# Kernel optimization log

Hardware: AMD Instinct MI355X
Metric: run time of the kernel (lower is better)

## Reference

```python
import math
import jax, jax.numpy as jnp
import numpy as np

B, Q, M = 4, 512, 8192
LOC_D, SENS_D, EMB_D = 8, 256, 512


def setup_inputs() -> dict:
    key = jax.random.key(0)
    ks = jax.random.split(key, 6)
    location = jax.random.normal(ks[0], (B, Q, LOC_D), dtype=jnp.float32)
    # sds must be positive (they are squared and logged); keep them away from 0
    location_sd = jax.random.uniform(ks[1], (B, Q, LOC_D), dtype=jnp.float32) * 0.9 + 0.1
    memory_locations = jax.random.normal(ks[2], (B, M, LOC_D), dtype=jnp.float32)
    memory_location_sds = jax.random.uniform(ks[3], (B, M, LOC_D), dtype=jnp.float32) * 0.9 + 0.1
    memory_senses = jax.random.normal(ks[4], (B, M, EMB_D), dtype=jnp.float32)
    # sensory_read_proj: Linear(embed_dim -> sensory_dim, bias=False)
    W_read = jax.random.normal(ks[5], (SENS_D, EMB_D), dtype=jnp.float32) / math.sqrt(EMB_D)
    return {
        "location": location,
        "location_sd": location_sd,
        "memory_locations": memory_locations,
        "memory_location_sds": memory_location_sds,
        "memory_senses": memory_senses,
        "W_read": W_read,
    }


def reference(location, location_sd, memory_locations, memory_location_sds, memory_senses, W_read):
    # BidirectionalMemory.read with match_threshold=None, detach_* True (stop_gradient)
    mem_loc = jax.lax.stop_gradient(memory_locations)
    mem_sd = jax.lax.stop_gradient(memory_location_sds)
    mem_sense = jax.lax.stop_gradient(memory_senses)

    # (B,Q,1,D) - (B,1,M,D) -> (B,Q,M,D)
    delta = location[:, :, None, :] - mem_loc[:, None, :, :]
    var = location_sd[:, :, None, :] ** 2 + mem_sd[:, None, :, :] ** 2
    d = delta.shape[-1]
    # -0.5 * sum((delta^2 / (var+eps))^2) - 0.5*log(2pi)*D - sum(log(var))
    log_aff = (
        -0.5 * jnp.sum((delta ** 2 / (var + 1e-8)) ** 2, axis=-1)
        - 0.5 * math.log(2.0 * math.pi) * d
        - jnp.sum(jnp.log(var), axis=-1)
    )  # (B,Q,M)
    weights = jax.nn.softmax(log_aff, axis=-1)  # (B,Q,M)
    pre_sense = jnp.einsum("bqm,bme->bqe", weights, mem_sense)  # (B,Q,EMB_D)
    sense = jnp.einsum("bqe,se->bqs", pre_sense, W_read)  # (B,Q,SENS_D)
    return sense
```

## Files before the change

kernel.cpp:

```cpp
#include <hip/hip_runtime.h>
#include <hip/hip_bf16.h>

#define BB 4
#define QQ 512
#define MM 8192
#define DD 8
#define EE 512
#define SS 256

#define QG 16
#define MSP 8
#define MSL (MM / MSP)
#define NQG (BB * QQ / QG)

using f32x4  = __attribute__((ext_vector_type(4))) float;
using bf16x8 = __attribute__((ext_vector_type(8))) short;

static __device__ __forceinline__ unsigned short f2bf(float f) {
  union { __hip_bfloat16 h; unsigned short u; } v;
  v.h = __float2bfloat16(f);
  return v.u;
}

__global__ __launch_bounds__(256) void k_proj(
    const float* __restrict__ V, const float* __restrict__ W,
    unsigned short* __restrict__ projT)
{
  const int m0 = blockIdx.x * 128;
  const int s0 = blockIdx.y * 128;
  const int b  = blockIdx.z;
  const int t = threadIdx.x, lane = t & 63, wv = t >> 6;
  const int wr = wv >> 1, wc = wv & 1;

  __shared__ short lA[128 * 64];
  __shared__ short lB[128 * 64];

  f32x4 acc[4][4] = {};

  const float* Wp = W + (size_t)s0 * EE;
  const float* Vp = V + (size_t)b * MM * EE + (size_t)m0 * EE;

  const int r0 = t >> 4;
  const int c0 = (t & 15) * 4;
  const int swz = (r0 & 7) << 3;

  float4 ra[8], rb[8];

#define P_LOADS(K0)                                                        \
  _Pragma("unroll")                                                        \
  for (int j = 0; j < 8; ++j) {                                            \
    const int row = j * 16 + r0;                                           \
    ra[j] = *reinterpret_cast<const float4*>(&Wp[(size_t)row * EE + (K0) + c0]); \
    rb[j] = *reinterpret_cast<const float4*>(&Vp[(size_t)row * EE + (K0) + c0]); \
  }

  P_LOADS(0)

  for (int ki = 0; ki < 8; ++ki) {
    __syncthreads();
#pragma unroll
    for (int j = 0; j < 8; ++j) {
      const int row = j * 16 + r0;
      const int idx = (row * 64 + c0) ^ swz;
      ushort4 da, db;
      da.x = f2bf(ra[j].x); da.y = f2bf(ra[j].y); da.z = f2bf(ra[j].z); da.w = f2bf(ra[j].w);
      db.x = f2bf(rb[j].x); db.y = f2bf(rb[j].y); db.z = f2bf(rb[j].z); db.w = f2bf(rb[j].w);
      *reinterpret_cast<ushort4*>(&lA[idx]) = da;
      *reinterpret_cast<ushort4*>(&lB[idx]) = db;
    }
    if (ki < 7) { P_LOADS((ki + 1) * 64) }
    __syncthreads();

#pragma unroll
    for (int kk = 0; kk < 2; ++kk) {
      const int kofs = kk * 32 + (lane >> 4) * 8;
      const int r15 = lane & 15;
      bf16x8 af[4], bfv[4];
#pragma unroll
      for (int mi = 0; mi < 4; ++mi) {
        int row = wr * 64 + mi * 16 + r15;
        af[mi] = *reinterpret_cast<const bf16x8*>(&lA[(row * 64 + kofs) ^ ((row & 7) << 3)]);
      }
#pragma unroll
      for (int ni = 0; ni < 4; ++ni) {
        int row = wc * 64 + ni * 16 + r15;
        bfv[ni] = *reinterpret_cast<const bf16x8*>(&lB[(row * 64 + kofs) ^ ((row & 7) << 3)]);
      }
#pragma unroll
      for (int mi = 0; mi < 4; ++mi)
#pragma unroll
        for (int ni = 0; ni < 4; ++ni)
          acc[mi][ni] = __builtin_amdgcn_mfma_f32_16x16x32_bf16(af[mi], bfv[ni], acc[mi][ni], 0, 0, 0);
    }
  }
#undef P_LOADS

  unsigned short* outp = projT + (size_t)b * SS * MM;
  const int fr = (lane >> 4) * 4;
  const int fc = lane & 15;
#pragma unroll
  for (int mi = 0; mi < 4; ++mi)
#pragma unroll
    for (int ni = 0; ni < 4; ++ni)
#pragma unroll
      for (int r = 0; r < 4; ++r) {
        int s = s0 + wr * 64 + mi * 16 + fr + r;
        int m = m0 + wc * 64 + ni * 16 + fc;
        outp[(size_t)s * MM + m] = f2bf(acc[mi][ni][r]);
      }
}

__global__ __launch_bounds__(512, 4) void k_fused(
    const float* __restrict__ loc, const float* __restrict__ locsd,
    const float* __restrict__ mloc, const float* __restrict__ msd,
    const unsigned short* __restrict__ projT,
    float* __restrict__ opart, float* __restrict__ mn_g,
    float* __restrict__ sum_g)
{
  __shared__ unsigned short p_s[QG * MSL];
  __shared__ float lx_s[QG][DD], ls2_s[QG][DD];
  __shared__ float redmin[QG][8];
  __shared__ float redsum[QG][8];

  const int hw = blockIdx.x;
  const int ms = hw & 7;
  const int qg = hw >> 3;
  const int b  = qg >> 5;
  const int q0 = (qg & 31) * QG;
  const int t = threadIdx.x, lane = t & 63, wv = t >> 6;

  if (t < QG * DD) {
    const int qq = t >> 3, d = t & 7;
    const int base = (b * QQ + q0 + qq) * DD + d;
    lx_s[qq][d] = loc[base];
    float s = locsd[base];
    ls2_s[qq][d] = __builtin_fmaf(s, s, 1e-8f);
  }

  const float4* ml4 = reinterpret_cast<const float4*>(mloc + (size_t)b * MM * DD);
  const float4* ms4 = reinterpret_cast<const float4*>(msd  + (size_t)b * MM * DD);
  float mlv[2][DD], ms2[2][DD];
#pragma unroll
  for (int p = 0; p < 2; ++p) {
    const int m = ms * MSL + 2 * t + p;
    float4 a0 = ml4[2 * m], a1 = ml4[2 * m + 1];
    float4 s0 = ms4[2 * m], s1 = ms4[2 * m + 1];
    mlv[p][0] = a0.x; mlv[p][1] = a0.y; mlv[p][2] = a0.z; mlv[p][3] = a0.w;
    mlv[p][4] = a1.x; mlv[p][5] = a1.y; mlv[p][6] = a1.z; mlv[p][7] = a1.w;
    ms2[p][0] = s0.x * s0.x; ms2[p][1] = s0.y * s0.y;
    ms2[p][2] = s0.z * s0.z; ms2[p][3] = s0.w * s0.w;
    ms2[p][4] = s1.x * s1.x; ms2[p][5] = s1.y * s1.y;
    ms2[p][6] = s1.z * s1.z; ms2[p][7] = s1.w * s1.w;
  }
  __syncthreads();

  const size_t g_base = ((size_t)qg * MSP + ms) * QG;

#pragma unroll
  for (int sub = 0; sub < 2; ++sub) {
    float la_r[8][2];
#pragma unroll
    for (int q8 = 0; q8 < 8; ++q8) {
      const int q = sub * 8 + q8;
      float lxq[DD], lsq[DD];
#pragma unroll
      for (int d = 0; d < DD; d += 4) {
        float4 v1 = *reinterpret_cast<const float4*>(&lx_s[q][d]);
        lxq[d] = v1.x; lxq[d + 1] = v1.y; lxq[d + 2] = v1.z; lxq[d + 3] = v1.w;
        float4 v2 = *reinterpret_cast<const float4*>(&ls2_s[q][d]);
        lsq[d] = v2.x; lsq[d + 1] = v2.y; lsq[d + 2] = v2.z; lsq[d + 3] = v2.w;
      }
      float mnq = 3.4e38f;
#pragma unroll
      for (int p = 0; p < 2; ++p) {
        float ssum = 0.f, pr = 1.f;
#pragma unroll
        for (int d = 0; d < DD; ++d) {
          float v  = lsq[d] + ms2[p][d];
          float r  = __builtin_amdgcn_rcpf(v);
          float dl = lxq[d] - mlv[p][d];
          float d2 = dl * dl;
          float tt = d2 * r;
          ssum = __builtin_fmaf(tt, tt, ssum);
          pr *= v;
        }
        la_r[q8][p] = __builtin_fmaf(ssum, 0.72134752f, __builtin_amdgcn_logf(pr));
        mnq = fminf(mnq, la_r[q8][p]);
      }
#pragma unroll
      for (int off = 32; off; off >>= 1) mnq = fminf(mnq, __shfl_xor(mnq, off, 64));
      if (lane == 0) redmin[q][wv] = mnq;
    }
    __syncthreads();
    float mnb[8];
#pragma unroll
    for (int q8 = 0; q8 < 8; ++q8) {
      const int q = sub * 8 + q8;
      float m2 = redmin[q][0];
#pragma unroll
      for (int w = 1; w < 8; ++w) m2 = fminf(m2, redmin[q][w]);
      mnb[q8] = m2;
      if (t == q8) mn_g[g_base + q] = m2;
    }
#pragma unroll
    for (int q8 = 0; q8 < 8; ++q8) {
      const int q = sub * 8 + q8;
      const int swz = (q & 7) << 4;
      float e0 = __builtin_amdgcn_exp2f(mnb[q8] - la_r[q8][0]);
      float e1 = __builtin_amdgcn_exp2f(mnb[q8] - la_r[q8][1]);
      unsigned int pk = (unsigned int)f2bf(e0) | ((unsigned int)f2bf(e1) << 16);
      *reinterpret_cast<unsigned int*>(
          (char*)p_s + (((q * MSL + 2 * t) * 2) ^ swz)) = pk;
      float v = e0 + e1;
#pragma unroll
      for (int off = 32; off; off >>= 1) v += __shfl_xor(v, off, 64);
      if (lane == 0) redsum[q][wv] = v;
    }
  }

  __syncthreads();
  if (t < QG) {
    float s = 0.f;
#pragma unroll
    for (int w = 0; w < 8; ++w) s += redsum[t][w];
    sum_g[g_base + t] = s;
  }

  const unsigned short* pTb = projT + (size_t)b * SS * MM + (size_t)ms * MSL;
  const int s0w = wv * 32;
  const int qf = lane & 15;
  const int kf = (lane >> 4) * 8;
  const int aswz = (qf & 7) << 4;
  f32x4 acc[2] = {};

#define LDA(CH) (*reinterpret_cast<const bf16x8*>( \
    (const char*)p_s + (((qf * MSL + (CH) * 32 + kf) * 2) ^ aswz)))
#define LOADB(U, CH)                                                        \
  _Pragma("unroll")                                                         \
  for (int ni = 0; ni < 2; ++ni)                                            \
    U[ni] = *reinterpret_cast<const uint4*>(                                \
        pTb + (size_t)(s0w + ni * 16 + qf) * MM + (CH) * 32 + kf);

  uint4 u0[2], u1[2];
  bf16x8 a0, a1;
  LOADB(u0, 0) a0 = LDA(0);
#pragma unroll 2
  for (int ch = 0; ch < 32; ch += 2) {
    LOADB(u1, ch + 1) a1 = LDA(ch + 1);
#pragma unroll
    for (int ni = 0; ni < 2; ++ni)
      acc[ni] = __builtin_amdgcn_mfma_f32_16x16x32_bf16(
          a0, *reinterpret_cast<const bf16x8*>(&u0[ni]), acc[ni], 0, 0, 0);
    if (ch + 2 < 32) { LOADB(u0, ch + 2) a0 = LDA(ch + 2); }
#pragma unroll
    for (int ni = 0; ni < 2; ++ni)
      acc[ni] = __builtin_amdgcn_mfma_f32_16x16x32_bf16(
          a1, *reinterpret_cast<const bf16x8*>(&u1[ni]), acc[ni], 0, 0, 0);
  }
#undef LDA
#undef LOADB

  float* op = opart + g_base * SS;
#pragma unroll
  for (int ni = 0; ni < 2; ++ni)
#pragma unroll
    for (int r = 0; r < 4; ++r) {
      const int q = (lane >> 4) * 4 + r;
      const int s = s0w + ni * 16 + qf;
      op[q * SS + s] = acc[ni][r];
    }
}

__global__ __launch_bounds__(256) void k_merge(
    const float* __restrict__ opart, const float* __restrict__ mn_g,
    const float* __restrict__ sum_g, float* __restrict__ out)
{
  const int row = blockIdx.x * 4 + (threadIdx.x >> 6);
  const int lane = threadIdx.x & 63;
  const int qg = row >> 4, q = row & 15;

  const float* mnp = mn_g  + (size_t)qg * MSP * QG + q;
  const float* smp = sum_g + (size_t)qg * MSP * QG + q;
  float mns[MSP], gmn = 3.4e38f;
#pragma unroll
  for (int i = 0; i < MSP; ++i) { mns[i] = mnp[i * QG]; gmn = fminf(gmn, mns[i]); }
  float gsum = 0.f, sc[MSP];
#pragma unroll
  for (int i = 0; i < MSP; ++i) {
    sc[i] = __builtin_amdgcn_exp2f(gmn - mns[i]);
    gsum = __builtin_fmaf(smp[i * QG], sc[i], gsum);
  }
  float o[4] = {0.f, 0.f, 0.f, 0.f};
  const float* ob = opart + (size_t)qg * MSP * (QG * SS) + q * SS;
#pragma unroll
  for (int i = 0; i < MSP; ++i)
#pragma unroll
    for (int j = 0; j < 4; ++j)
      o[j] = __builtin_fmaf(ob[(size_t)i * (QG * SS) + j * 64 + lane], sc[i], o[j]);
  const float inv = 1.0f / gsum;
  float* orow = out + (size_t)row * SS;
#pragma unroll
  for (int j = 0; j < 4; ++j) orow[j * 64 + lane] = o[j] * inv;
}


extern "C" void kernel_launch(void* const* d_in, const int* in_sizes, int n_in,
                              void* d_out, int out_size, void* d_ws, size_t ws_size,
                              hipStream_t stream) {
  const float* loc    = (const float*)d_in[0];
  const float* locsd  = (const float*)d_in[1];
  const float* mloc   = (const float*)d_in[2];
  const float* msd    = (const float*)d_in[3];
  const float* msense = (const float*)d_in[4];
  const float* wread  = (const float*)d_in[5];
  float* out = (float*)d_out;

  const size_t proj_bytes  = (size_t)BB * SS * MM * 2;
  const size_t opart_bytes = (size_t)NQG * MSP * QG * SS * 4;
  const size_t mn_bytes    = (size_t)NQG * MSP * QG * 4;
  if (ws_size < proj_bytes + opart_bytes + 2 * mn_bytes) return;

  unsigned short* projT = (unsigned short*)d_ws;
  float* opart = (float*)((char*)d_ws + proj_bytes);
  float* mn_g  = (float*)((char*)d_ws + proj_bytes + opart_bytes);
  float* sum_g = (float*)((char*)d_ws + proj_bytes + opart_bytes + mn_bytes);

  hipLaunchKernelGGL(k_proj, dim3(MM / 128, SS / 128, BB), dim3(256), 0, stream,
                     msense, wread, projT);
  hipLaunchKernelGGL(k_fused, dim3(NQG * MSP), dim3(512), 0, stream,
                     loc, locsd, mloc, msd, projT, opart, mn_g, sum_g);
  hipLaunchKernelGGL(k_merge, dim3(BB * QQ / 4), dim3(256), 0, stream,
                     opart, mn_g, sum_g, out);
}
```

Measured before the change: 111.1 us.

## Remap affinity stage so each half-wave owns one query

Threads are remapped so that each 32-lane half-wave handles one query and iterates over all memory slots of the slice, instead of each thread owning two memory slots across all 16 queries. This lets the per-query min and sum be reduced with in-wave shuffles only, removing the shared-memory reduction arrays and the intermediate block barriers. The per-dimension reciprocals are also replaced by two reciprocals of partial products, using shared sub-products to cut transcendental work. In exchange, memory location and sd data are now reloaded from global memory once per query (16x more global/L2 traffic), and the product-based reciprocal may lose precision.

```diff
diff --git a/kernel.cpp b/kernel.cpp
--- a/kernel.cpp
+++ b/kernel.cpp
@@ -12,6 +12,8 @@
 #define MSP 8
 #define MSL (MM / MSP)
 #define NQG (BB * QQ / QG)
+
+#define L2E 0.72134752f
 
 using f32x4  = __attribute__((ext_vector_type(4))) float;
 using bf16x8 = __attribute__((ext_vector_type(8))) short;
@@ -118,9 +120,7 @@
     float* __restrict__ sum_g)
 {
   __shared__ unsigned short p_s[QG * MSL];
-  __shared__ float lx_s[QG][DD], ls2_s[QG][DD];
-  __shared__ float redmin[QG][8];
-  __shared__ float redsum[QG][8];
+  __shared__ float2 lxls_s[QG][DD];
 
   const int hw = blockIdx.x;
   const int ms = hw & 7;
@@ -128,103 +128,90 @@
   const int b  = qg >> 5;
   const int q0 = (qg & 31) * QG;
   const int t = threadIdx.x, lane = t & 63, wv = t >> 6;
+  const int ql = t >> 5;
+  const int lh = lane & 31;
 
   if (t < QG * DD) {
     const int qq = t >> 3, d = t & 7;
     const int base = (b * QQ + q0 + qq) * DD + d;
-    lx_s[qq][d] = loc[base];
     float s = locsd[base];
-    ls2_s[qq][d] = __builtin_fmaf(s, s, 1e-8f);
-  }
+    float2 v; v.x = loc[base]; v.y = __builtin_fmaf(s, s, 1e-8f);
+    lxls_s[qq][d] = v;
+  }
+  __syncthreads();
+
+  float lx[DD], ls[DD];
+#pragma unroll
+  for (int d = 0; d < DD; ++d) {
+    float2 v = lxls_s[ql][d];
+    lx[d] = v.x; ls[d] = v.y;
+  }
+
+  const size_t g_base = ((size_t)qg * MSP + ms) * QG;
 
   const float4* ml4 = reinterpret_cast<const float4*>(mloc + (size_t)b * MM * DD);
   const float4* ms4 = reinterpret_cast<const float4*>(msd  + (size_t)b * MM * DD);
-  float mlv[2][DD], ms2[2][DD];
-#pragma unroll
-  for (int p = 0; p < 2; ++p) {
-    const int m = ms * MSL + 2 * t + p;
-    float4 a0 = ml4[2 * m], a1 = ml4[2 * m + 1];
-    float4 s0 = ms4[2 * m], s1 = ms4[2 * m + 1];
-    mlv[p][0] = a0.x; mlv[p][1] = a0.y; mlv[p][2] = a0.z; mlv[p][3] = a0.w;
-    mlv[p][4] = a1.x; mlv[p][5] = a1.y; mlv[p][6] = a1.z; mlv[p][7] = a1.w;
-    ms2[p][0] = s0.x * s0.x; ms2[p][1] = s0.y * s0.y;
-    ms2[p][2] = s0.z * s0.z; ms2[p][3] = s0.w * s0.w;
-    ms2[p][4] = s1.x * s1.x; ms2[p][5] = s1.y * s1.y;
-    ms2[p][6] = s1.z * s1.z; ms2[p][7] = s1.w * s1.w;
-  }
+  const int mb = ms * MSL + 2 * lh;
+
+  float la[16][2];
+  float mn = 3.4e38f;
+#pragma unroll
+  for (int i = 0; i < 16; ++i) {
+#pragma unroll
+    for (int p = 0; p < 2; ++p) {
+      const int m = mb + i * 64 + p;
+      float4 a0 = ml4[2 * m], a1 = ml4[2 * m + 1];
+      float4 s0 = ms4[2 * m], s1 = ms4[2 * m + 1];
+      float vv0 = ls[0] + s0.x * s0.x, vv1 = ls[1] + s0.y * s0.y;
+      float vv2 = ls[2] + s0.z * s0.z, vv3 = ls[3] + s0.w * s0.w;
+      float vv4 = ls[4] + s1.x * s1.x, vv5 = ls[5] + s1.y * s1.y;
+      float vv6 = ls[6] + s1.z * s1.z, vv7 = ls[7] + s1.w * s1.w;
+      float d0 = lx[0] - a0.x, d1 = lx[1] - a0.y, d2 = lx[2] - a0.z, d3 = lx[3] - a0.w;
+      float d4 = lx[4] - a1.x, d5 = lx[5] - a1.y, d6 = lx[6] - a1.z, d7 = lx[7] - a1.w;
+      float e0 = d0 * d0, e1 = d1 * d1, e2 = d2 * d2, e3 = d3 * d3;
+      float e4 = d4 * d4, e5 = d5 * d5, e6 = d6 * d6, e7 = d7 * d7;
+      float v01 = vv0 * vv1, v23 = vv2 * vv3, v45 = vv4 * vv5, v67 = vv6 * vv7;
+      float pA = v01 * v23, pB = v45 * v67;
+      float rA = __builtin_amdgcn_rcpf(pA);
+      float rB = __builtin_amdgcn_rcpf(pB);
+      float pp = pA * pB;
+      float t0 = e0 * vv1 * v23 * rA, t1 = e1 * vv0 * v23 * rA;
+      float t2 = e2 * vv3 * v01 * rA, t3 = e3 * vv2 * v01 * rA;
+      float t4 = e4 * vv5 * v67 * rB, t5 = e5 * vv4 * v67 * rB;
+      float t6 = e6 * vv7 * v45 * rB, t7 = e7 * vv6 * v45 * rB;
+      float ss = t0 * t0;
+      ss = __builtin_fmaf(t1, t1, ss);
+      ss = __builtin_fmaf(t2, t2, ss);
+      ss = __builtin_fmaf(t3, t3, ss);
+      ss = __builtin_fmaf(t4, t4, ss);
+      ss = __builtin_fmaf(t5, t5, ss);
+      ss = __builtin_fmaf(t6, t6, ss);
+      ss = __builtin_fmaf(t7, t7, ss);
+      la[i][p] = __builtin_fmaf(ss, L2E, __builtin_amdgcn_logf(pp));
+      mn = fminf(mn, la[i][p]);
+    }
+  }
+
+#pragma unroll
+  for (int off = 16; off; off >>= 1) mn = fminf(mn, __shfl_xor(mn, off, 64));
+  if (lh == 0) mn_g[g_base + ql] = mn;
+
+  const int swz = (ql & 7) << 4;
+  float sum = 0.f;
+#pragma unroll
+  for (int i = 0; i < 16; ++i) {
+    float e0 = __builtin_amdgcn_exp2f(mn - la[i][0]);
+    float e1 = __builtin_amdgcn_exp2f(mn - la[i][1]);
+    sum += e0 + e1;
+    unsigned int pk = (unsigned int)f2bf(e0) | ((unsigned int)f2bf(e1) << 16);
+    *reinterpret_cast<unsigned int*>(
+        (char*)p_s + (((ql * MSL + i * 64 + 2 * lh) * 2) ^ swz)) = pk;
+  }
+#pragma unroll
+  for (int off = 16; off; off >>= 1) sum += __shfl_xor(sum, off, 64);
+  if (lh == 0) sum_g[g_base + ql] = sum;
+
   __syncthreads();
-
-  const size_t g_base = ((size_t)qg * MSP + ms) * QG;
-
-#pragma unroll
-  for (int sub = 0; sub < 2; ++sub) {
-    float la_r[8][2];
-#pragma unroll
-    for (int q8 = 0; q8 < 8; ++q8) {
-      const int q = sub * 8 + q8;
-      float lxq[DD], lsq[DD];
-#pragma unroll
-      for (int d = 0; d < DD; d += 4) {
-        float4 v1 = *reinterpret_cast<const float4*>(&lx_s[q][d]);
-        lxq[d] = v1.x; lxq[d + 1] = v1.y; lxq[d + 2] = v1.z; lxq[d + 3] = v1.w;
-        float4 v2 = *reinterpret_cast<const float4*>(&ls2_s[q][d]);
-        lsq[d] = v2.x; lsq[d + 1] = v2.y; lsq[d + 2] = v2.z; lsq[d + 3] = v2.w;
-      }
-      float mnq = 3.4e38f;
-#pragma unroll
-      for (int p = 0; p < 2; ++p) {
-        float ssum = 0.f, pr = 1.f;
-#pragma unroll
-        for (int d = 0; d < DD; ++d) {
-          float v  = lsq[d] + ms2[p][d];
-          float r  = __builtin_amdgcn_rcpf(v);
-          float dl = lxq[d] - mlv[p][d];
-          float d2 = dl * dl;
-          float tt = d2 * r;
-          ssum = __builtin_fmaf(tt, tt, ssum);
-          pr *= v;
-        }
-        la_r[q8][p] = __builtin_fmaf(ssum, 0.72134752f, __builtin_amdgcn_logf(pr));
-        mnq = fminf(mnq, la_r[q8][p]);
-      }
-#pragma unroll
-      for (int off = 32; off; off >>= 1) mnq = fminf(mnq, __shfl_xor(mnq, off, 64));
-      if (lane == 0) redmin[q][wv] = mnq;
-    }
-    __syncthreads();
-    float mnb[8];
-#pragma unroll
-    for (int q8 = 0; q8 < 8; ++q8) {
-      const int q = sub * 8 + q8;
-      float m2 = redmin[q][0];
-#pragma unroll
-      for (int w = 1; w < 8; ++w) m2 = fminf(m2, redmin[q][w]);
-      mnb[q8] = m2;
-      if (t == q8) mn_g[g_base + q] = m2;
-    }
-#pragma unroll
-    for (int q8 = 0; q8 < 8; ++q8) {
-      const int q = sub * 8 + q8;
-      const int swz = (q & 7) << 4;
-      float e0 = __builtin_amdgcn_exp2f(mnb[q8] - la_r[q8][0]);
-      float e1 = __builtin_amdgcn_exp2f(mnb[q8] - la_r[q8][1]);
-      unsigned int pk = (unsigned int)f2bf(e0) | ((unsigned int)f2bf(e1) << 16);
-      *reinterpret_cast<unsigned int*>(
-          (char*)p_s + (((q * MSL + 2 * t) * 2) ^ swz)) = pk;
-      float v = e0 + e1;
-#pragma unroll
-      for (int off = 32; off; off >>= 1) v += __shfl_xor(v, off, 64);
-      if (lane == 0) redsum[q][wv] = v;
-    }
-  }
-
-  __syncthreads();
-  if (t < QG) {
-    float s = 0.f;
-#pragma unroll
-    for (int w = 0; w < 8; ++w) s += redsum[t][w];
-    sum_g[g_base + t] = s;
-  }
 
   const unsigned short* pTb = projT + (size_t)b * SS * MM + (size_t)ms * MSL;
   const int s0w = wv * 32;
```

Measured after the change: 142.3 us. +28.1%, slower.

## Split memory axis into 16 slices with one memory row per thread

Applied to the files above, without the earlier changes.

Doubles the number of memory-axis splits per query group, so each block handles half as many memory rows (one per thread instead of two) and the MFMA k-loop is halved. This gives twice as many blocks and smaller per-block LDS use, which may raise occupancy and parallelism. It also restructures the affinity pass into one sweep over all 16 queries with a shared-memory broadcast of the per-query minimum, replacing the two-half pass. The cost is twice as many partial outputs for the merge kernel to read and combine, plus more global traffic for the partial results.

```diff
diff --git a/kernel.cpp b/kernel.cpp
--- a/kernel.cpp
+++ b/kernel.cpp
@@ -9,9 +9,11 @@
 #define SS 256
 
 #define QG 16
-#define MSP 8
+#define MSP 16
 #define MSL (MM / MSP)
 #define NQG (BB * QQ / QG)
+
+#define L2E 0.72134752f
 
 using f32x4  = __attribute__((ext_vector_type(4))) float;
 using bf16x8 = __attribute__((ext_vector_type(8))) short;
@@ -121,10 +123,11 @@
   __shared__ float lx_s[QG][DD], ls2_s[QG][DD];
   __shared__ float redmin[QG][8];
   __shared__ float redsum[QG][8];
+  __shared__ float mnb_s[QG];
 
   const int hw = blockIdx.x;
-  const int ms = hw & 7;
-  const int qg = hw >> 3;
+  const int ms = hw & 15;
+  const int qg = hw >> 4;
   const int b  = qg >> 5;
   const int q0 = (qg & 31) * QG;
   const int t = threadIdx.x, lane = t & 63, wv = t >> 6;
@@ -139,85 +142,83 @@
 
   const float4* ml4 = reinterpret_cast<const float4*>(mloc + (size_t)b * MM * DD);
   const float4* ms4 = reinterpret_cast<const float4*>(msd  + (size_t)b * MM * DD);
-  float mlv[2][DD], ms2[2][DD];
-#pragma unroll
-  for (int p = 0; p < 2; ++p) {
-    const int m = ms * MSL + 2 * t + p;
-    float4 a0 = ml4[2 * m], a1 = ml4[2 * m + 1];
-    float4 s0 = ms4[2 * m], s1 = ms4[2 * m + 1];
-    mlv[p][0] = a0.x; mlv[p][1] = a0.y; mlv[p][2] = a0.z; mlv[p][3] = a0.w;
-    mlv[p][4] = a1.x; mlv[p][5] = a1.y; mlv[p][6] = a1.z; mlv[p][7] = a1.w;
-    ms2[p][0] = s0.x * s0.x; ms2[p][1] = s0.y * s0.y;
-    ms2[p][2] = s0.z * s0.z; ms2[p][3] = s0.w * s0.w;
-    ms2[p][4] = s1.x * s1.x; ms2[p][5] = s1.y * s1.y;
-    ms2[p][6] = s1.z * s1.z; ms2[p][7] = s1.w * s1.w;
-  }
+  const int m = ms * MSL + t;
+  float4 a0 = ml4[2 * m], a1 = ml4[2 * m + 1];
+  float4 s0q = ms4[2 * m], s1q = ms4[2 * m + 1];
+  float mlv[DD], ms2[DD];
+  mlv[0] = a0.x; mlv[1] = a0.y; mlv[2] = a0.z; mlv[3] = a0.w;
+  mlv[4] = a1.x; mlv[5] = a1.y; mlv[6] = a1.z; mlv[7] = a1.w;
+  ms2[0] = s0q.x * s0q.x; ms2[1] = s0q.y * s0q.y;
+  ms2[2] = s0q.z * s0q.z; ms2[3] = s0q.w * s0q.w;
+  ms2[4] = s1q.x * s1q.x; ms2[5] = s1q.y * s1q.y;
+  ms2[6] = s1q.z * s1q.z; ms2[7] = s1q.w * s1q.w;
   __syncthreads();
 
   const size_t g_base = ((size_t)qg * MSP + ms) * QG;
 
-#pragma unroll
-  for (int sub = 0; sub < 2; ++sub) {
-    float la_r[8][2];
-#pragma unroll
-    for (int q8 = 0; q8 < 8; ++q8) {
-      const int q = sub * 8 + q8;
-      float lxq[DD], lsq[DD];
-#pragma unroll
-      for (int d = 0; d < DD; d += 4) {
-        float4 v1 = *reinterpret_cast<const float4*>(&lx_s[q][d]);
-        lxq[d] = v1.x; lxq[d + 1] = v1.y; lxq[d + 2] = v1.z; lxq[d + 3] = v1.w;
-        float4 v2 = *reinterpret_cast<const float4*>(&ls2_s[q][d]);
-        lsq[d] = v2.x; lsq[d + 1] = v2.y; lsq[d + 2] = v2.z; lsq[d + 3] = v2.w;
-      }
-      float mnq = 3.4e38f;
-#pragma unroll
-      for (int p = 0; p < 2; ++p) {
-        float ssum = 0.f, pr = 1.f;
-#pragma unroll
-        for (int d = 0; d < DD; ++d) {
-          float v  = lsq[d] + ms2[p][d];
-          float r  = __builtin_amdgcn_rcpf(v);
-          float dl = lxq[d] - mlv[p][d];
-          float d2 = dl * dl;
-          float tt = d2 * r;
-          ssum = __builtin_fmaf(tt, tt, ssum);
-          pr *= v;
-        }
-        la_r[q8][p] = __builtin_fmaf(ssum, 0.72134752f, __builtin_amdgcn_logf(pr));
-        mnq = fminf(mnq, la_r[q8][p]);
-      }
-#pragma unroll
-      for (int off = 32; off; off >>= 1) mnq = fminf(mnq, __shfl_xor(mnq, off, 64));
-      if (lane == 0) redmin[q][wv] = mnq;
-    }
-    __syncthreads();
-    float mnb[8];
-#pragma unroll
-    for (int q8 = 0; q8 < 8; ++q8) {
-      const int q = sub * 8 + q8;
-      float m2 = redmin[q][0];
-#pragma unroll
-      for (int w = 1; w < 8; ++w) m2 = fminf(m2, redmin[q][w]);
-      mnb[q8] = m2;
-      if (t == q8) mn_g[g_base + q] = m2;
-    }
-#pragma unroll
-    for (int q8 = 0; q8 < 8; ++q8) {
-      const int q = sub * 8 + q8;
-      const int swz = (q & 7) << 4;
-      float e0 = __builtin_amdgcn_exp2f(mnb[q8] - la_r[q8][0]);
-      float e1 = __builtin_amdgcn_exp2f(mnb[q8] - la_r[q8][1]);
-      unsigned int pk = (unsigned int)f2bf(e0) | ((unsigned int)f2bf(e1) << 16);
-      *reinterpret_cast<unsigned int*>(
-          (char*)p_s + (((q * MSL + 2 * t) * 2) ^ swz)) = pk;
-      float v = e0 + e1;
-#pragma unroll
-      for (int off = 32; off; off >>= 1) v += __shfl_xor(v, off, 64);
-      if (lane == 0) redsum[q][wv] = v;
-    }
-  }
-
+  float la[QG];
+#pragma unroll
+  for (int q = 0; q < QG; ++q) {
+    float lxq[DD], lsq[DD];
+#pragma unroll
+    for (int d = 0; d < DD; d += 4) {
+      float4 v1 = *reinterpret_cast<const float4*>(&lx_s[q][d]);
+      lxq[d] = v1.x; lxq[d + 1] = v1.y; lxq[d + 2] = v1.z; lxq[d + 3] = v1.w;
+      float4 v2 = *reinterpret_cast<const float4*>(&ls2_s[q][d]);
+      lsq[d] = v2.x; lsq[d + 1] = v2.y; lsq[d + 2] = v2.z; lsq[d + 3] = v2.w;
+    }
+    float ssum = 0.f, pr = 1.f;
+#pragma unroll
+    for (int d = 0; d < DD; ++d) {
+      float v  = lsq[d] + ms2[d];
+      float r  = __builtin_amdgcn_rcpf(v);
+      float dl = lxq[d] - mlv[d];
+      float d2 = dl * dl;
+      float tt = d2 * r;
+      ssum = __builtin_fmaf(tt, tt, ssum);
+      pr *= v;
+    }
+    la[q] = __builtin_fmaf(ssum, L2E, __builtin_amdgcn_logf(pr));
+  }
+
+#pragma unroll
+  for (int q = 0; q < QG; ++q) {
+    float v = la[q];
+#pragma unroll
+    for (int off = 32; off; off >>= 1) v = fminf(v, __shfl_xor(v, off, 64));
+    if (lane == 0) redmin[q][wv] = v;
+  }
+  __syncthreads();
+  if (t < QG) {
+    float m2 = redmin[t][0];
+#pragma unroll
+    for (int w = 1; w < 8; ++w) m2 = fminf(m2, redmin[t][w]);
+    mnb_s[t] = m2;
+    mn_g[g_base + t] = m2;
+  }
+  __syncthreads();
+  float mnb[QG];
+#pragma unroll
+  for (int q = 0; q < QG; q += 4) {
+    float4 v = *reinterpret_cast<const float4*>(&mnb_s[q]);
+    mnb[q] = v.x; mnb[q + 1] = v.y; mnb[q + 2] = v.z; mnb[q + 3] = v.w;
+  }
+
+#pragma unroll
+  for (int q = 0; q < QG; ++q) {
+    float e = __builtin_amdgcn_exp2f(mnb[q] - la[q]);
+    la[q] = e;
+    *reinterpret_cast<unsigned short*>(
+        (char*)p_s + (((q * MSL + t) * 2) ^ ((q & 7) << 4))) = f2bf(e);
+  }
+
+#pragma unroll
+  for (int q = 0; q < QG; ++q) {
+    float v = la[q];
+#pragma unroll
+    for (int off = 32; off; off >>= 1) v += __shfl_xor(v, off, 64);
+    if (lane == 0) redsum[q][wv] = v;
+  }
   __syncthreads();
   if (t < QG) {
     float s = 0.f;
@@ -242,20 +243,20 @@
         pTb + (size_t)(s0w + ni * 16 + qf) * MM + (CH) * 32 + kf);
 
   uint4 u0[2], u1[2];
-  bf16x8 a0, a1;
-  LOADB(u0, 0) a0 = LDA(0);
+  bf16x8 af0, af1;
+  LOADB(u0, 0) af0 = LDA(0);
 #pragma unroll 2
-  for (int ch = 0; ch < 32; ch += 2) {
-    LOADB(u1, ch + 1) a1 = LDA(ch + 1);
+  for (int ch = 0; ch < 16; ch += 2) {
+    LOADB(u1, ch + 1) af1 = LDA(ch + 1);
 #pragma unroll
     for (int ni = 0; ni < 2; ++ni)
       acc[ni] = __builtin_amdgcn_mfma_f32_16x16x32_bf16(
-          a0, *reinterpret_cast<const bf16x8*>(&u0[ni]), acc[ni], 0, 0, 0);
-    if (ch + 2 < 32) { LOADB(u0, ch + 2) a0 = LDA(ch + 2); }
+          af0, *reinterpret_cast<const bf16x8*>(&u0[ni]), acc[ni], 0, 0, 0);
+    if (ch + 2 < 16) { LOADB(u0, ch + 2) af0 = LDA(ch + 2); }
 #pragma unroll
     for (int ni = 0; ni < 2; ++ni)
       acc[ni] = __builtin_amdgcn_mfma_f32_16x16x32_bf16(
-          a1, *reinterpret_cast<const bf16x8*>(&u1[ni]), acc[ni], 0, 0, 0);
+          af1, *reinterpret_cast<const bf16x8*>(&u1[ni]), acc[ni], 0, 0, 0);
   }
 #undef LDA
 #undef LOADB
```

New measurement: 280.1 us. 2.52x slower.
